# Performance work log

Hardware: AMD Instinct MI355X
Metric: run time of the kernel (lower is better)

Reference implementation:

```python
import jax, jax.numpy as jnp
import numpy as np

N = 100000
E = 3200000
F_IN = 128
H = 64
NUM_GRAPHS = 256


def setup_inputs() -> dict:
    key = jax.random.key(0)
    ks = jax.random.split(key, 8)
    x = jax.random.normal(ks[0], (N, F_IN), dtype=jnp.float32)
    edge_index = jax.random.randint(ks[1], (2, E), 0, N, dtype=jnp.int32)
    batch = jnp.sort(jax.random.randint(ks[2], (N,), 0, NUM_GRAPHS, dtype=jnp.int32))
    # Glorot-ish init for weights
    W1 = jax.random.normal(ks[3], (F_IN, H), dtype=jnp.float32) / np.sqrt(F_IN)
    b1 = jnp.zeros((H,), dtype=jnp.float32)
    W2 = jax.random.normal(ks[4], (H, H), dtype=jnp.float32) / np.sqrt(H)
    b2 = jnp.zeros((H,), dtype=jnp.float32)
    Wfc = jax.random.normal(ks[5], (H, 1), dtype=jnp.float32) / np.sqrt(H)
    bfc = jnp.zeros((1,), dtype=jnp.float32)
    return {"x": x, "edge_index": edge_index, "batch": batch,
            "W1": W1, "b1": b1, "W2": W2, "b2": b2, "Wfc": Wfc, "bfc": bfc}


def reference(x, edge_index, batch, W1, b1, W2, b2, Wfc, bfc):
    n = x.shape[0]
    loops = jnp.arange(n, dtype=edge_index.dtype)
    # GCN adds self-loops, then symmetric degree normalization
    src = jnp.concatenate([edge_index[0], loops])  # message sources
    dst = jnp.concatenate([edge_index[1], loops])  # message targets
    deg = jax.ops.segment_sum(jnp.ones_like(dst, dtype=x.dtype), dst, num_segments=n)
    d_inv_sqrt = jnp.where(deg > 0, jax.lax.rsqrt(deg), 0.0)
    norm = d_inv_sqrt[src] * d_inv_sqrt[dst]  # [E+N]

    def gcn_conv(h, W, b):
        hw = h @ W                                   # [N, H] small GEMM
        msg = hw[src] * norm[:, None]                # gather + scale  [E+N, H]
        agg = jax.ops.segment_sum(msg, dst, num_segments=n)  # scatter-add
        return agg + b

    h = jax.nn.relu(gcn_conv(x, W1, b1))
    h = jax.nn.relu(gcn_conv(h, W2, b2))

    # global_mean_pool over graphs in the batch
    pooled = jax.ops.segment_sum(h, batch, num_segments=NUM_GRAPHS)
    counts = jax.ops.segment_sum(jnp.ones((n,), dtype=h.dtype), batch, num_segments=NUM_GRAPHS)
    mean = pooled / jnp.maximum(counts, 1.0)[:, None]

    return mean @ Wfc + bfc  # [NUM_GRAPHS, 1]
```

## Files before the change

### kernel.cpp

```cpp
#include <hip/hip_runtime.h>

#define F_IN 128
#define HDIM 64
#define NUM_GRAPHS 256
#define SCAN_BLK 256
#define SCAN_CHUNK 2048

__global__ void hist_kernel(const int* __restrict__ dst, int* __restrict__ deg, int e) {
    int i = blockIdx.x * blockDim.x + threadIdx.x;
    if (i < e) atomicAdd(&deg[dst[i]], 1);
}

__global__ void scan_partial(const int* __restrict__ deg, int* __restrict__ partial, int n) {
    __shared__ int lds[SCAN_BLK];
    int b = blockIdx.x, t = threadIdx.x;
    int base = b * SCAN_CHUNK + t * 8;
    int s = 0;
#pragma unroll
    for (int j = 0; j < 8; ++j) { int idx = base + j; if (idx < n) s += deg[idx]; }
    lds[t] = s; __syncthreads();
    for (int off = SCAN_BLK / 2; off; off >>= 1) {
        if (t < off) lds[t] += lds[t + off];
        __syncthreads();
    }
    if (t == 0) partial[b] = lds[0];
}

__global__ void scan_spine(int* __restrict__ partial, int nb, int* __restrict__ off_end) {
    if (threadIdx.x == 0 && blockIdx.x == 0) {
        int run = 0;
        for (int i = 0; i < nb; ++i) { int v = partial[i]; partial[i] = run; run += v; }
        off_end[0] = run;
    }
}

__global__ void scan_final(const int* __restrict__ deg, const int* __restrict__ partial,
                           int* __restrict__ off, int* __restrict__ cursor,
                           float* __restrict__ dinv, int n) {
    __shared__ int lds[SCAN_BLK];
    int b = blockIdx.x, t = threadIdx.x;
    int base = b * SCAN_CHUNK + t * 8;
    int v[8]; int s = 0;
#pragma unroll
    for (int j = 0; j < 8; ++j) { int idx = base + j; v[j] = (idx < n) ? deg[idx] : 0; s += v[j]; }
    lds[t] = s; __syncthreads();
    for (int o = 1; o < SCAN_BLK; o <<= 1) {
        int y = (t >= o) ? lds[t - o] : 0;
        __syncthreads();
        if (t >= o) lds[t] += y;
        __syncthreads();
    }
    int run = partial[b] + lds[t] - s;
#pragma unroll
    for (int j = 0; j < 8; ++j) {
        int idx = base + j;
        if (idx < n) {
            off[idx] = run; cursor[idx] = run;
            dinv[idx] = rsqrtf((float)v[j] + 1.0f);
        }
        run += v[j];
    }
}

__global__ void fill_kernel(const int* __restrict__ src, const int* __restrict__ dst,
                            int* __restrict__ cursor, int* __restrict__ csr, int e) {
    int i = blockIdx.x * blockDim.x + threadIdx.x;
    if (i < e) {
        int pos = atomicAdd(&cursor[dst[i]], 1);
        csr[pos] = src[i];
    }
}

template<int K>
__global__ void gemm_kernel(const float* __restrict__ A, const float* __restrict__ W,
                            const float* __restrict__ dinv, float* __restrict__ out, int n) {
    __shared__ float Ws[K * 64];
    for (int i = threadIdx.x; i < K * 64; i += blockDim.x) Ws[i] = W[i];
    __syncthreads();
    int row  = blockIdx.x * (blockDim.x >> 6) + (threadIdx.x >> 6);
    int lane = threadIdx.x & 63;
    if (row >= n) return;
    const float4* ar = reinterpret_cast<const float4*>(A + (size_t)row * K);
    float acc = 0.f;
#pragma unroll
    for (int k4 = 0; k4 < K / 4; ++k4) {
        float4 av = ar[k4];
        acc = fmaf(av.x, Ws[(k4 * 4 + 0) * 64 + lane], acc);
        acc = fmaf(av.y, Ws[(k4 * 4 + 1) * 64 + lane], acc);
        acc = fmaf(av.z, Ws[(k4 * 4 + 2) * 64 + lane], acc);
        acc = fmaf(av.w, Ws[(k4 * 4 + 3) * 64 + lane], acc);
    }
    out[(size_t)row * 64 + lane] = acc * dinv[row];
}

template<bool POOL>
__global__ void gather_kernel(const int* __restrict__ off, const int* __restrict__ csr,
                              const float* __restrict__ hws, const float* __restrict__ dinv,
                              const float* __restrict__ b, const int* __restrict__ batch,
                              float* __restrict__ hout, float* __restrict__ pooled,
                              float* __restrict__ cnt, int n) {
    int d = blockIdx.x * (blockDim.x >> 6) + (threadIdx.x >> 6);
    int lane = threadIdx.x & 63;
    if (d >= n) return;
    int beg = off[d], end = off[d + 1];
    float acc[8];
#pragma unroll
    for (int j = 0; j < 8; ++j) acc[j] = 0.f;

    for (int base = beg; base < end; base += 64) {
        int m = end - base; if (m > 64) m = 64;
        int myidx = (lane < m) ? csr[base + lane] : 0;
        int i = 0;
        for (; i + 8 <= m; i += 8) {
#pragma unroll
            for (int j = 0; j < 8; ++j) {
                int s = __shfl(myidx, i + j);
                acc[j] += hws[(size_t)s * 64 + lane];
            }
        }
        for (; i < m; ++i) {
            int s = __shfl(myidx, i);
            acc[i & 7] += hws[(size_t)s * 64 + lane];
        }
    }
    float tot = ((acc[0] + acc[1]) + (acc[2] + acc[3])) +
                ((acc[4] + acc[5]) + (acc[6] + acc[7]));
    float v = (tot + hws[(size_t)d * 64 + lane]) * dinv[d] + b[lane];
    v = fmaxf(v, 0.f);
    if (POOL) {
        int g = batch[d];
        atomicAdd(&pooled[(size_t)g * 64 + lane], v);
        if (lane == 0) atomicAdd(&cnt[g], 1.0f);
    } else {
        hout[(size_t)d * 64 + lane] = v;
    }
}

__global__ void final_kernel(const float* __restrict__ pooled, const float* __restrict__ cnt,
                             const float* __restrict__ Wfc, const float* __restrict__ bfc,
                             float* __restrict__ out) {
    int g = blockIdx.x;
    int lane = threadIdx.x;
    float c = fmaxf(cnt[g], 1.0f);
    float v = (pooled[(size_t)g * 64 + lane] / c) * Wfc[lane];
#pragma unroll
    for (int off = 32; off; off >>= 1) v += __shfl_down(v, off);
    if (lane == 0) out[g] = v + bfc[0];
}

extern "C" void kernel_launch(void* const* d_in, const int* in_sizes, int n_in,
                              void* d_out, int out_size, void* d_ws, size_t ws_size,
                              hipStream_t stream) {
    const float* x    = (const float*)d_in[0];
    const int*   ei   = (const int*)d_in[1];
    const int*   batch= (const int*)d_in[2];
    const float* W1   = (const float*)d_in[3];
    const float* b1   = (const float*)d_in[4];
    const float* W2   = (const float*)d_in[5];
    const float* b2   = (const float*)d_in[6];
    const float* Wfc  = (const float*)d_in[7];
    const float* bfc  = (const float*)d_in[8];
    float* out = (float*)d_out;

    const int n = in_sizes[0] / F_IN;
    const int e = in_sizes[1] / 2;
    const int* srcp = ei;
    const int* dstp = ei + e;

    size_t nAl = ((size_t)n + 256) & ~(size_t)255;
    int*   deg     = (int*)d_ws;
    int*   off     = deg + nAl;
    int*   cursor  = off + nAl;
    int*   partial = cursor + nAl;
    float* dinv    = (float*)(partial + 256);
    int*   csr     = (int*)(dinv + nAl);
    size_t eAl     = ((size_t)e + 255) & ~(size_t)255;
    float* hws     = (float*)(csr + eAl);
    float* h1      = hws + (size_t)n * 64;
    float* pooled  = h1 + (size_t)n * 64;
    float* cnt     = pooled + (size_t)NUM_GRAPHS * 64;

    const int nb = (n + SCAN_CHUNK - 1) / SCAN_CHUNK;

    hipMemsetAsync(deg, 0, (size_t)n * sizeof(int), stream);
    hist_kernel<<<(e + 255) / 256, 256, 0, stream>>>(dstp, deg, e);
    scan_partial<<<nb, SCAN_BLK, 0, stream>>>(deg, partial, n);
    scan_spine<<<1, 64, 0, stream>>>(partial, nb, &off[n]);
    scan_final<<<nb, SCAN_BLK, 0, stream>>>(deg, partial, off, cursor, dinv, n);
    fill_kernel<<<(e + 255) / 256, 256, 0, stream>>>(srcp, dstp, cursor, csr, e);

    gemm_kernel<F_IN><<<(n + 3) / 4, 256, 0, stream>>>(x, W1, dinv, hws, n);
    gather_kernel<false><<<(n + 3) / 4, 256, 0, stream>>>(off, csr, hws, dinv, b1, batch,
                                                          h1, nullptr, nullptr, n);

    gemm_kernel<HDIM><<<(n + 3) / 4, 256, 0, stream>>>(h1, W2, dinv, hws, n);
    hipMemsetAsync(pooled, 0, ((size_t)NUM_GRAPHS * 64 + NUM_GRAPHS) * sizeof(float), stream);
    gather_kernel<true><<<(n + 3) / 4, 256, 0, stream>>>(off, csr, hws, dinv, b2, batch,
                                                         nullptr, pooled, cnt, n);

    final_kernel<<<NUM_GRAPHS, 64, 0, stream>>>(pooled, cnt, Wfc, bfc, out);
}
```

Baseline: 1.253 ms.

## Store intermediate node features in fp16 and gather two edges per wavefront

The transformed features hws and the hidden layer h1 are now stored as half precision, and accumulation stays in fp32. The gather kernel splits each 64-lane wavefront into two halves that each read a different neighbour's 32 half2 columns, then combines them with a cross-half shuffle. This halves the bytes moved by the random-access neighbour gathers, which dominate the runtime, at the cost of fp16 rounding error in the intermediate activations.

```diff
diff --git a/kernel.cpp b/kernel.cpp
--- a/kernel.cpp
+++ b/kernel.cpp
@@ -1,4 +1,5 @@
 #include <hip/hip_runtime.h>
+#include <hip/hip_fp16.h>
 
 #define F_IN 128
 #define HDIM 64
@@ -71,68 +72,104 @@
     }
 }
 
-template<int K>
-__global__ void gemm_kernel(const float* __restrict__ A, const float* __restrict__ W,
-                            const float* __restrict__ dinv, float* __restrict__ out, int n) {
-    __shared__ float Ws[K * 64];
-    for (int i = threadIdx.x; i < K * 64; i += blockDim.x) Ws[i] = W[i];
+__global__ void gemm1_kernel(const float* __restrict__ A, const float* __restrict__ W,
+                             const float* __restrict__ dinv, __half* __restrict__ out, int n) {
+    __shared__ float Ws[F_IN * 64];
+    for (int i = threadIdx.x; i < F_IN * 64; i += blockDim.x) Ws[i] = W[i];
     __syncthreads();
     int row  = blockIdx.x * (blockDim.x >> 6) + (threadIdx.x >> 6);
     int lane = threadIdx.x & 63;
     if (row >= n) return;
-    const float4* ar = reinterpret_cast<const float4*>(A + (size_t)row * K);
+    const float4* ar = reinterpret_cast<const float4*>(A + (size_t)row * F_IN);
     float acc = 0.f;
 #pragma unroll
-    for (int k4 = 0; k4 < K / 4; ++k4) {
+    for (int k4 = 0; k4 < F_IN / 4; ++k4) {
         float4 av = ar[k4];
         acc = fmaf(av.x, Ws[(k4 * 4 + 0) * 64 + lane], acc);
         acc = fmaf(av.y, Ws[(k4 * 4 + 1) * 64 + lane], acc);
         acc = fmaf(av.z, Ws[(k4 * 4 + 2) * 64 + lane], acc);
         acc = fmaf(av.w, Ws[(k4 * 4 + 3) * 64 + lane], acc);
     }
-    out[(size_t)row * 64 + lane] = acc * dinv[row];
+    out[(size_t)row * 64 + lane] = __float2half(acc * dinv[row]);
+}
+
+__global__ void gemm2_kernel(const __half* __restrict__ A, const float* __restrict__ W,
+                             const float* __restrict__ dinv, __half* __restrict__ out, int n) {
+    __shared__ float Ws[HDIM * 64];
+    for (int i = threadIdx.x; i < HDIM * 64; i += blockDim.x) Ws[i] = W[i];
+    __syncthreads();
+    int row  = blockIdx.x * (blockDim.x >> 6) + (threadIdx.x >> 6);
+    int lane = threadIdx.x & 63;
+    if (row >= n) return;
+    const __half2* ar = reinterpret_cast<const __half2*>(A + (size_t)row * HDIM);
+    float acc = 0.f;
+#pragma unroll
+    for (int k2 = 0; k2 < HDIM / 2; ++k2) {
+        float2 av = __half22float2(ar[k2]);
+        acc = fmaf(av.x, Ws[(k2 * 2 + 0) * 64 + lane], acc);
+        acc = fmaf(av.y, Ws[(k2 * 2 + 1) * 64 + lane], acc);
+    }
+    out[(size_t)row * 64 + lane] = __float2half(acc * dinv[row]);
 }
 
 template<bool POOL>
 __global__ void gather_kernel(const int* __restrict__ off, const int* __restrict__ csr,
-                              const float* __restrict__ hws, const float* __restrict__ dinv,
+                              const __half2* __restrict__ hws, const float* __restrict__ dinv,
                               const float* __restrict__ b, const int* __restrict__ batch,
-                              float* __restrict__ hout, float* __restrict__ pooled,
+                              __half* __restrict__ hout, float* __restrict__ pooled,
                               float* __restrict__ cnt, int n) {
     int d = blockIdx.x * (blockDim.x >> 6) + (threadIdx.x >> 6);
     int lane = threadIdx.x & 63;
     if (d >= n) return;
+    int half_id = lane >> 5;
+    int col = lane & 31;
     int beg = off[d], end = off[d + 1];
-    float acc[8];
-#pragma unroll
-    for (int j = 0; j < 8; ++j) acc[j] = 0.f;
+    float2 acc[8];
+#pragma unroll
+    for (int j = 0; j < 8; ++j) { acc[j].x = 0.f; acc[j].y = 0.f; }
 
     for (int base = beg; base < end; base += 64) {
         int m = end - base; if (m > 64) m = 64;
         int myidx = (lane < m) ? csr[base + lane] : 0;
         int i = 0;
-        for (; i + 8 <= m; i += 8) {
+        for (; i + 16 <= m; i += 16) {
 #pragma unroll
             for (int j = 0; j < 8; ++j) {
-                int s = __shfl(myidx, i + j);
-                acc[j] += hws[(size_t)s * 64 + lane];
+                int s = __shfl(myidx, i + 2 * j + half_id);
+                float2 f = __half22float2(hws[(size_t)s * 32 + col]);
+                acc[j].x += f.x; acc[j].y += f.y;
             }
         }
-        for (; i < m; ++i) {
-            int s = __shfl(myidx, i);
-            acc[i & 7] += hws[(size_t)s * 64 + lane];
+        for (; i < m; i += 4) {
+#pragma unroll
+            for (int j = 0; j < 2; ++j) {
+                int e2 = i + 2 * j + half_id;
+                int s = __shfl(myidx, (e2 < m) ? e2 : 0);
+                float2 f = __half22float2(hws[(size_t)s * 32 + col]);
+                if (e2 < m) { acc[j].x += f.x; acc[j].y += f.y; }
+            }
         }
     }
-    float tot = ((acc[0] + acc[1]) + (acc[2] + acc[3])) +
-                ((acc[4] + acc[5]) + (acc[6] + acc[7]));
-    float v = (tot + hws[(size_t)d * 64 + lane]) * dinv[d] + b[lane];
-    v = fmaxf(v, 0.f);
+    float2 tot;
+    tot.x = ((acc[0].x + acc[1].x) + (acc[2].x + acc[3].x)) +
+            ((acc[4].x + acc[5].x) + (acc[6].x + acc[7].x));
+    tot.y = ((acc[0].y + acc[1].y) + (acc[2].y + acc[3].y)) +
+            ((acc[4].y + acc[5].y) + (acc[6].y + acc[7].y));
+    tot.x += __shfl_xor(tot.x, 32);
+    tot.y += __shfl_xor(tot.y, 32);
+    float2 self = __half22float2(hws[(size_t)d * 32 + col]);
+    float di = dinv[d];
+    float2 bb = reinterpret_cast<const float2*>(b)[col];
+    float vx = fmaxf((tot.x + self.x) * di + bb.x, 0.f);
+    float vy = fmaxf((tot.y + self.y) * di + bb.y, 0.f);
+    float vsel = half_id ? vy : vx;
+    int feat = 2 * col + half_id;
     if (POOL) {
         int g = batch[d];
-        atomicAdd(&pooled[(size_t)g * 64 + lane], v);
+        atomicAdd(&pooled[(size_t)g * 64 + feat], vsel);
         if (lane == 0) atomicAdd(&cnt[g], 1.0f);
     } else {
-        hout[(size_t)d * 64 + lane] = v;
+        hout[(size_t)d * 64 + feat] = __float2half(vsel);
     }
 }
 
@@ -168,17 +205,17 @@
     const int* dstp = ei + e;
 
     size_t nAl = ((size_t)n + 256) & ~(size_t)255;
-    int*   deg     = (int*)d_ws;
-    int*   off     = deg + nAl;
-    int*   cursor  = off + nAl;
-    int*   partial = cursor + nAl;
-    float* dinv    = (float*)(partial + 256);
-    int*   csr     = (int*)(dinv + nAl);
-    size_t eAl     = ((size_t)e + 255) & ~(size_t)255;
-    float* hws     = (float*)(csr + eAl);
-    float* h1      = hws + (size_t)n * 64;
-    float* pooled  = h1 + (size_t)n * 64;
-    float* cnt     = pooled + (size_t)NUM_GRAPHS * 64;
+    int*    deg     = (int*)d_ws;
+    int*    off     = deg + nAl;
+    int*    cursor  = off + nAl;
+    int*    partial = cursor + nAl;
+    float*  dinv    = (float*)(partial + 256);
+    int*    csr     = (int*)(dinv + nAl);
+    size_t  eAl     = ((size_t)e + 255) & ~(size_t)255;
+    __half* hws     = (__half*)(csr + eAl);
+    __half* h1      = hws + (size_t)n * 64;
+    float*  pooled  = (float*)(h1 + (size_t)n * 64);
+    float*  cnt     = pooled + (size_t)NUM_GRAPHS * 64;
 
     const int nb = (n + SCAN_CHUNK - 1) / SCAN_CHUNK;
 
@@ -189,14 +226,16 @@
     scan_final<<<nb, SCAN_BLK, 0, stream>>>(deg, partial, off, cursor, dinv, n);
     fill_kernel<<<(e + 255) / 256, 256, 0, stream>>>(srcp, dstp, cursor, csr, e);
 
-    gemm_kernel<F_IN><<<(n + 3) / 4, 256, 0, stream>>>(x, W1, dinv, hws, n);
-    gather_kernel<false><<<(n + 3) / 4, 256, 0, stream>>>(off, csr, hws, dinv, b1, batch,
-                                                          h1, nullptr, nullptr, n);
-
-    gemm_kernel<HDIM><<<(n + 3) / 4, 256, 0, stream>>>(h1, W2, dinv, hws, n);
+    gemm1_kernel<<<(n + 3) / 4, 256, 0, stream>>>(x, W1, dinv, hws, n);
+    gather_kernel<false><<<(n + 3) / 4, 256, 0, stream>>>(off, csr, (const __half2*)hws,
+                                                          dinv, b1, batch, h1,
+                                                          nullptr, nullptr, n);
+
+    gemm2_kernel<<<(n + 3) / 4, 256, 0, stream>>>(h1, W2, dinv, hws, n);
     hipMemsetAsync(pooled, 0, ((size_t)NUM_GRAPHS * 64 + NUM_GRAPHS) * sizeof(float), stream);
-    gather_kernel<true><<<(n + 3) / 4, 256, 0, stream>>>(off, csr, hws, dinv, b2, batch,
-                                                         nullptr, pooled, cnt, n);
+    gather_kernel<true><<<(n + 3) / 4, 256, 0, stream>>>(off, csr, (const __half2*)hws,
+                                                         dinv, b2, batch, nullptr,
+                                                         pooled, cnt, n);
 
     final_kernel<<<NUM_GRAPHS, 64, 0, stream>>>(pooled, cnt, Wfc, bfc, out);
 }
```

After: 1.318 ms. +5.2%, slower.
